# Kernel optimization log

Measured on AMD Instinct MI355X. Metric: run time of the kernel, lower is better.

Reference implementation:

```python
import jax, jax.numpy as jnp
import numpy as np

BINS = 10
LOSS_WEIGHT = 1.0


def setup_inputs() -> dict:
    key = jax.random.key(0)
    k1, k2 = jax.random.split(key)
    B, C = 16384, 1000
    logits = jax.random.normal(k1, (B, C), dtype=jnp.float32)
    target_indices = jax.random.randint(k2, (B,), 0, C)
    return {"logits": logits, "target_indices": target_indices}


def reference(logits, target_indices):
    B, C = logits.shape
    bins = BINS
    target = jax.nn.one_hot(target_indices, C, dtype=logits.dtype)  # [B, C]
    # gradient-norm proxy (detached in the original)
    g = jnp.abs(jax.nn.sigmoid(jax.lax.stop_gradient(logits)) - target)  # [B, C], in [0, 1]
    tot = jnp.asarray(B * C, logits.dtype)  # all label_weights are 1 -> tot = B*C
    # edges are i/bins with last edge bumped by 1e-6, so bin = clip(floor(g*bins), 0, bins-1)
    bin_idx = jnp.clip((g * bins).astype(jnp.int32), 0, bins - 1)  # [B, C]
    counts = jax.ops.segment_sum(
        jnp.ones((B * C,), logits.dtype), bin_idx.reshape(-1), num_segments=bins
    )  # [bins]
    nonempty = counts > 0
    n = jnp.sum(nonempty).astype(logits.dtype)  # number of non-empty bins
    per_bin_w = jnp.where(nonempty, tot / jnp.maximum(counts, 1.0), 0.0)  # [bins]
    weights = per_bin_w[bin_idx] / jnp.maximum(n, 1.0)  # [B, C]
    weights = jax.lax.stop_gradient(weights)
    # binary_cross_entropy_with_logits, elementwise, stable form
    bce = jnp.maximum(logits, 0.0) - logits * target + jnp.log1p(jnp.exp(-jnp.abs(logits)))
    loss = jnp.sum(weights * bce) / tot
    return loss * LOSS_WEIGHT
```

## Files before the change

kernel.cpp:

```cpp
#include <hip/hip_runtime.h>

typedef float v2f __attribute__((ext_vector_type(2)));

namespace {
constexpr int kB = 16384;
constexpr int kC = 1000;
constexpr int kNElem = kB * kC;
constexpr int kNV8 = kNElem / 8;
constexpr int kV8PerRow = kC / 8;
constexpr int kBlocks = 1280;
constexpr int kThreads = 256;
constexpr int kStride = kBlocks * kThreads;
}


__device__ __forceinline__ void ghmc_elem(float L, float& bce, unsigned& bin)
{
    const float kLn2   = 0.6931471805599453f;
    const float kNRLn2 = -1.4426950408889634f;
    const float en  = __builtin_amdgcn_exp2f(kNRLn2 * fabsf(L));
    const float den = 1.f + en;
    const float lg  = __builtin_amdgcn_logf(den);
    const float r   = __builtin_amdgcn_rcpf(den);
    bce = fmaf(lg, kLn2, fmaxf(L, 0.f));
    unsigned babs = (unsigned)(10.f * r);
    babs = babs > 9u ? 9u : babs;
    bin = (L >= 0.f) ? babs : 9u - babs;
}

__device__ __forceinline__ void proc4(const float4 v,
    v2f& a01, v2f& a23, v2f& a45, v2f& a67, v2f& a89,
    unsigned long long& hcnt,
    const v2f C01, const v2f C23, const v2f C45, const v2f C67, const v2f C89)
{
    const float lv[4] = {v.x, v.y, v.z, v.w};
    #pragma unroll
    for (int e = 0; e < 4; ++e) {
        float bce; unsigned bin;
        ghmc_elem(lv[e], bce, bin);
        hcnt += 1ull << (6u * bin);
        const v2f b2 = {bce, bce};
        a01 += __builtin_elementwise_max(b2, C01);
        a23 += __builtin_elementwise_max(b2, C23);
        a45 += __builtin_elementwise_max(b2, C45);
        a67 += __builtin_elementwise_max(b2, C67);
        a89 += __builtin_elementwise_max(b2, C89);
    }
}

__global__ __launch_bounds__(kThreads) void ghmc_main(
    const float* __restrict__ logits,
    const int* __restrict__ tgt,
    float* __restrict__ pf,
    unsigned* __restrict__ pu)
{
    const v2f C01 = {0.0f,        0.10536052f};
    const v2f C23 = {0.22314355f, 0.35667494f};
    const v2f C45 = {0.51082562f, 0.69314718f};
    const v2f C67 = {0.91629073f, 1.20397280f};
    const v2f C89 = {1.60943791f, 2.30258509f};

    v2f a01 = {0.f,0.f}, a23 = {0.f,0.f}, a45 = {0.f,0.f},
        a67 = {0.f,0.f}, a89 = {0.f,0.f};
    unsigned long long hcnt = 0ull;

    const int gid = blockIdx.x * blockDim.x + threadIdx.x;
    const int n = (kNV8 - 1 - gid) / kStride + 1;
    const float4* __restrict__ Lp = reinterpret_cast<const float4*>(logits);

    int i = gid;
    int ib = i + kStride;     if (ib >= kNV8) ib = kNV8 - 1;
    float4 a0 = Lp[2 * i],  a1 = Lp[2 * i + 1];
    float4 b0 = Lp[2 * ib], b1 = Lp[2 * ib + 1];

    for (int k = 0; k < n; ++k) {
        int ic = i + 2 * kStride; if (ic >= kNV8) ic = kNV8 - 1;
        const float4 c0 = Lp[2 * ic], c1 = Lp[2 * ic + 1];

        const int row = i / kV8PerRow;
        const int dt  = tgt[row] - (i - row * kV8PerRow) * 8;

        proc4(a0, a01, a23, a45, a67, a89, hcnt, C01, C23, C45, C67, C89);
        proc4(a1, a01, a23, a45, a67, a89, hcnt, C01, C23, C45, C67, C89);

        if (__builtin_expect((unsigned)dt < 8u, 0)) {
            float L = a0.x;
            L = (dt == 1) ? a0.y : L;
            L = (dt == 2) ? a0.z : L;
            L = (dt == 3) ? a0.w : L;
            L = (dt == 4) ? a1.x : L;
            L = (dt == 5) ? a1.y : L;
            L = (dt == 6) ? a1.z : L;
            L = (dt == 7) ? a1.w : L;
            float bn_; unsigned bnb;
            ghmc_elem(L, bn_, bnb);
            const float bt_ = bn_ - L;
            unsigned babs = (bnb >= 5u) ? bnb : 9u - bnb;
            const unsigned btb = (L <= 0.f) ? babs : 9u - babs;
            hcnt += (1ull << (6u * btb)) - (1ull << (6u * bnb));
            const v2f bn2 = {bn_, bn_}, bt2 = {bt_, bt_};
            a01 += __builtin_elementwise_max(bt2, C01) - __builtin_elementwise_max(bn2, C01);
            a23 += __builtin_elementwise_max(bt2, C23) - __builtin_elementwise_max(bn2, C23);
            a45 += __builtin_elementwise_max(bt2, C45) - __builtin_elementwise_max(bn2, C45);
            a67 += __builtin_elementwise_max(bt2, C67) - __builtin_elementwise_max(bn2, C67);
            a89 += __builtin_elementwise_max(bt2, C89) - __builtin_elementwise_max(bn2, C89);
        }

        a0 = b0; a1 = b1; b0 = c0; b1 = c1;
        i += kStride;
    }

    unsigned long long lo = 0ull, hi = 0ull;
    #pragma unroll
    for (int k = 0; k < 5; ++k) {
        lo += ((hcnt >> (6 * k))       & 63ull) << (12 * k);
        hi += ((hcnt >> (6 * (k + 5))) & 63ull) << (12 * k);
    }
    float r10[10] = {a01.x, a01.y, a23.x, a23.y, a45.x, a45.y, a67.x, a67.y, a89.x, a89.y};
    #pragma unroll
    for (int off = 32; off > 0; off >>= 1) {
        #pragma unroll
        for (int k = 0; k < 10; ++k) r10[k] += __shfl_down(r10[k], off);
        lo += __shfl_down(lo, off);
        hi += __shfl_down(hi, off);
    }

    __shared__ float              sf[4][10];
    __shared__ unsigned long long sc[4][2];
    const int wave = threadIdx.x >> 6;
    const int lane = threadIdx.x & 63;
    if (lane == 0) {
        #pragma unroll
        for (int k = 0; k < 10; ++k) sf[wave][k] = r10[k];
        sc[wave][0] = lo; sc[wave][1] = hi;
    }
    __syncthreads();
    const int t = threadIdx.x;
    if (t < 10) {
        pf[t * kBlocks + blockIdx.x] = sf[0][t] + sf[1][t] + sf[2][t] + sf[3][t];
    } else if (t < 20) {
        const int b = t - 10;
        const int half = (b < 5) ? 0 : 1;
        const int sh = 12 * (b < 5 ? b : b - 5);
        unsigned s = 0;
        #pragma unroll
        for (int w = 0; w < 4; ++w) s += (unsigned)((sc[w][half] >> sh) & 4095ull);
        pu[b * kBlocks + blockIdx.x] = s;
    }
}

__global__ __launch_bounds__(640) void ghmc_reduce(
    const float* __restrict__ pf,
    const unsigned* __restrict__ pu,
    float* __restrict__ out)
{
    const int wave = threadIdx.x >> 6;
    const int lane = threadIdx.x & 63;

    double   fs = 0.0;
    unsigned cs = 0u;
    for (int b = lane; b < kBlocks; b += 64) {
        fs += (double)pf[wave * kBlocks + b];
        cs += pu[wave * kBlocks + b];
    }
    #pragma unroll
    for (int off = 32; off > 0; off >>= 1) {
        fs += __shfl_down(fs, off);
        cs += __shfl_down(cs, off);
    }

    __shared__ double   sF[10];
    __shared__ unsigned sC[10];
    if (lane == 0) { sF[wave] = fs; sC[wave] = cs; }
    __syncthreads();

    if (threadIdx.x == 0) {
        const double cj[10] = {0.0,
            0.10536051565782630, 0.22314355131420976, 0.35667494393873245,
            0.51082562376599072, 0.69314718055994531, 0.91629073187415511,
            1.20397280432593600, 1.60943791243410040, 2.30258509299404570};
        double N[10], cnt[11], cum[11];
        for (int k = 0; k < 10; ++k) N[k] = (double)sC[k];
        cnt[10] = 0.0;
        for (int j = 9; j >= 0; --j) cnt[j] = cnt[j + 1] + N[j];
        cum[10] = 0.0;
        cum[0] = sF[0];
        for (int j = 1; j <= 9; ++j)
            cum[j] = sF[j] - cj[j] * ((double)kNElem - cnt[j]);
        double loss = 0.0, n = 0.0;
        for (int k = 0; k < 10; ++k) {
            if (N[k] > 0.0) { n += 1.0; loss += (cum[k] - cum[k + 1]) / N[k]; }
        }
        out[0] = (float)(loss / (n > 1.0 ? n : 1.0));
    }
}

extern "C" void kernel_launch(void* const* d_in, const int* in_sizes, int n_in,
                              void* d_out, int out_size, void* d_ws, size_t ws_size,
                              hipStream_t stream)
{
    const float* logits = (const float*)d_in[0];
    const int*   tgt    = (const int*)d_in[1];
    float*    pf = (float*)d_ws;
    unsigned* pu = (unsigned*)((char*)d_ws + 10 * kBlocks * 4);
    ghmc_main<<<kBlocks, kThreads, 0, stream>>>(logits, tgt, pf, pu);
    ghmc_reduce<<<1, 640, 0, stream>>>(pf, pu, (float*)d_out);
}
```

Measured before the change: 37.23 us.

## Switch to one coalesced float4 per lane with a deeper prefetch pipeline

The main loop now handles a single float4 per thread per grid-stride step instead of two adjacent float4s. Neighbouring lanes therefore read contiguous 16-byte chunks, and a three-deep register prefetch ring with a 4x unrolled loop keeps more loads in flight. The target-column check moves into the per-float4 routine, so the row and target lookup now runs twice as often. The final reduction kernel also switches to vectorized float4/uint4 loads with a fixed unrolled trip count.

```diff
diff --git a/kernel.cpp b/kernel.cpp
--- a/kernel.cpp
+++ b/kernel.cpp
@@ -6,11 +6,11 @@
 constexpr int kB = 16384;
 constexpr int kC = 1000;
 constexpr int kNElem = kB * kC;
-constexpr int kNV8 = kNElem / 8;
-constexpr int kV8PerRow = kC / 8;
+constexpr int kNV4 = kNElem / 4;
+constexpr int kV4PerRow = kC / 4;
 constexpr int kBlocks = 1280;
 constexpr int kThreads = 256;
-constexpr int kStride = kBlocks * kThreads;
+constexpr int kS = kBlocks * kThreads;
 }
 
 
@@ -28,7 +28,7 @@
     bin = (L >= 0.f) ? babs : 9u - babs;
 }
 
-__device__ __forceinline__ void proc4(const float4 v,
+__device__ __forceinline__ void proc4(const float4 v, int dt,
     v2f& a01, v2f& a23, v2f& a45, v2f& a67, v2f& a89,
     unsigned long long& hcnt,
     const v2f C01, const v2f C23, const v2f C45, const v2f C67, const v2f C89)
@@ -46,6 +46,30 @@
         a67 += __builtin_elementwise_max(b2, C67);
         a89 += __builtin_elementwise_max(b2, C89);
     }
+    if (__builtin_expect((unsigned)dt < 4u, 0)) {
+        float L = v.x;
+        L = (dt == 1) ? v.y : L;
+        L = (dt == 2) ? v.z : L;
+        L = (dt == 3) ? v.w : L;
+        float bn_; unsigned bnb;
+        ghmc_elem(L, bn_, bnb);
+        const float bt_ = bn_ - L;
+        const unsigned babs = (bnb >= 5u) ? bnb : 9u - bnb;
+        const unsigned btb  = (L <= 0.f) ? babs : 9u - babs;
+        hcnt += (1ull << (6u * btb)) - (1ull << (6u * bnb));
+        const v2f bn2 = {bn_, bn_}, bt2 = {bt_, bt_};
+        a01 += __builtin_elementwise_max(bt2, C01) - __builtin_elementwise_max(bn2, C01);
+        a23 += __builtin_elementwise_max(bt2, C23) - __builtin_elementwise_max(bn2, C23);
+        a45 += __builtin_elementwise_max(bt2, C45) - __builtin_elementwise_max(bn2, C45);
+        a67 += __builtin_elementwise_max(bt2, C67) - __builtin_elementwise_max(bn2, C67);
+        a89 += __builtin_elementwise_max(bt2, C89) - __builtin_elementwise_max(bn2, C89);
+    }
+}
+
+__device__ __forceinline__ int dt_for(const int* __restrict__ tgt, int i)
+{
+    const int row = i / kV4PerRow;
+    return tgt[row] - (i - row * kV4PerRow) * 4;
 }
 
 __global__ __launch_bounds__(kThreads) void ghmc_main(
@@ -65,62 +89,46 @@
     unsigned long long hcnt = 0ull;
 
     const int gid = blockIdx.x * blockDim.x + threadIdx.x;
-    const int n = (kNV8 - 1 - gid) / kStride + 1;
+    const int n = (kNV4 - 1 - gid) / kS + 1;
     const float4* __restrict__ Lp = reinterpret_cast<const float4*>(logits);
 
+    auto ld = [&](int idx) {
+        idx = idx < kNV4 ? idx : kNV4 - 1;
+        return Lp[idx];
+    };
+
     int i = gid;
-    int ib = i + kStride;     if (ib >= kNV8) ib = kNV8 - 1;
-    float4 a0 = Lp[2 * i],  a1 = Lp[2 * i + 1];
-    float4 b0 = Lp[2 * ib], b1 = Lp[2 * ib + 1];
-
-    for (int k = 0; k < n; ++k) {
-        int ic = i + 2 * kStride; if (ic >= kNV8) ic = kNV8 - 1;
-        const float4 c0 = Lp[2 * ic], c1 = Lp[2 * ic + 1];
-
-        const int row = i / kV8PerRow;
-        const int dt  = tgt[row] - (i - row * kV8PerRow) * 8;
-
-        proc4(a0, a01, a23, a45, a67, a89, hcnt, C01, C23, C45, C67, C89);
-        proc4(a1, a01, a23, a45, a67, a89, hcnt, C01, C23, C45, C67, C89);
-
-        if (__builtin_expect((unsigned)dt < 8u, 0)) {
-            float L = a0.x;
-            L = (dt == 1) ? a0.y : L;
-            L = (dt == 2) ? a0.z : L;
-            L = (dt == 3) ? a0.w : L;
-            L = (dt == 4) ? a1.x : L;
-            L = (dt == 5) ? a1.y : L;
-            L = (dt == 6) ? a1.z : L;
-            L = (dt == 7) ? a1.w : L;
-            float bn_; unsigned bnb;
-            ghmc_elem(L, bn_, bnb);
-            const float bt_ = bn_ - L;
-            unsigned babs = (bnb >= 5u) ? bnb : 9u - bnb;
-            const unsigned btb = (L <= 0.f) ? babs : 9u - babs;
-            hcnt += (1ull << (6u * btb)) - (1ull << (6u * bnb));
-            const v2f bn2 = {bn_, bn_}, bt2 = {bt_, bt_};
-            a01 += __builtin_elementwise_max(bt2, C01) - __builtin_elementwise_max(bn2, C01);
-            a23 += __builtin_elementwise_max(bt2, C23) - __builtin_elementwise_max(bn2, C23);
-            a45 += __builtin_elementwise_max(bt2, C45) - __builtin_elementwise_max(bn2, C45);
-            a67 += __builtin_elementwise_max(bt2, C67) - __builtin_elementwise_max(bn2, C67);
-            a89 += __builtin_elementwise_max(bt2, C89) - __builtin_elementwise_max(bn2, C89);
-        }
-
-        a0 = b0; a1 = b1; b0 = c0; b1 = c1;
-        i += kStride;
+    float4 q0 = ld(i), q1 = ld(i + kS), q2 = ld(i + 2 * kS);
+
+    int k = 0;
+    for (; k + 4 <= n; k += 4) {
+        float4 q3 = ld(i + 3 * kS);
+        proc4(q0, dt_for(tgt, i),          a01, a23, a45, a67, a89, hcnt, C01, C23, C45, C67, C89);
+        q0 = ld(i + 4 * kS);
+        proc4(q1, dt_for(tgt, i + kS),     a01, a23, a45, a67, a89, hcnt, C01, C23, C45, C67, C89);
+        q1 = ld(i + 5 * kS);
+        proc4(q2, dt_for(tgt, i + 2 * kS), a01, a23, a45, a67, a89, hcnt, C01, C23, C45, C67, C89);
+        q2 = ld(i + 6 * kS);
+        proc4(q3, dt_for(tgt, i + 3 * kS), a01, a23, a45, a67, a89, hcnt, C01, C23, C45, C67, C89);
+        i += 4 * kS;
+    }
+    for (; k < n; ++k) {
+        proc4(q0, dt_for(tgt, i), a01, a23, a45, a67, a89, hcnt, C01, C23, C45, C67, C89);
+        q0 = q1; q1 = q2;
+        i += kS;
     }
 
     unsigned long long lo = 0ull, hi = 0ull;
     #pragma unroll
-    for (int k = 0; k < 5; ++k) {
-        lo += ((hcnt >> (6 * k))       & 63ull) << (12 * k);
-        hi += ((hcnt >> (6 * (k + 5))) & 63ull) << (12 * k);
+    for (int j = 0; j < 5; ++j) {
+        lo += ((hcnt >> (6 * j))       & 63ull) << (12 * j);
+        hi += ((hcnt >> (6 * (j + 5))) & 63ull) << (12 * j);
     }
     float r10[10] = {a01.x, a01.y, a23.x, a23.y, a45.x, a45.y, a67.x, a67.y, a89.x, a89.y};
     #pragma unroll
     for (int off = 32; off > 0; off >>= 1) {
         #pragma unroll
-        for (int k = 0; k < 10; ++k) r10[k] += __shfl_down(r10[k], off);
+        for (int j = 0; j < 10; ++j) r10[j] += __shfl_down(r10[j], off);
         lo += __shfl_down(lo, off);
         hi += __shfl_down(hi, off);
     }
@@ -131,7 +139,7 @@
     const int lane = threadIdx.x & 63;
     if (lane == 0) {
         #pragma unroll
-        for (int k = 0; k < 10; ++k) sf[wave][k] = r10[k];
+        for (int j = 0; j < 10; ++j) sf[wave][j] = r10[j];
         sc[wave][0] = lo; sc[wave][1] = hi;
     }
     __syncthreads();
@@ -157,11 +165,16 @@
     const int wave = threadIdx.x >> 6;
     const int lane = threadIdx.x & 63;
 
+    const float4* pf4 = reinterpret_cast<const float4*>(pf + wave * kBlocks);
+    const uint4*  pu4 = reinterpret_cast<const uint4*>(pu + wave * kBlocks);
     double   fs = 0.0;
     unsigned cs = 0u;
-    for (int b = lane; b < kBlocks; b += 64) {
-        fs += (double)pf[wave * kBlocks + b];
-        cs += pu[wave * kBlocks + b];
+    #pragma unroll
+    for (int it = 0; it < kBlocks / 256; ++it) {
+        const float4 f = pf4[lane + it * 64];
+        const uint4  u = pu4[lane + it * 64];
+        fs += (double)f.x + (double)f.y + (double)f.z + (double)f.w;
+        cs += u.x + u.y + u.z + u.w;
     }
     #pragma unroll
     for (int off = 32; off > 0; off >>= 1) {
@@ -180,7 +193,7 @@
             0.51082562376599072, 0.69314718055994531, 0.91629073187415511,
             1.20397280432593600, 1.60943791243410040, 2.30258509299404570};
         double N[10], cnt[11], cum[11];
-        for (int k = 0; k < 10; ++k) N[k] = (double)sC[k];
+        for (int j = 0; j < 10; ++j) N[j] = (double)sC[j];
         cnt[10] = 0.0;
         for (int j = 9; j >= 0; --j) cnt[j] = cnt[j + 1] + N[j];
         cum[10] = 0.0;
@@ -188,8 +201,8 @@
         for (int j = 1; j <= 9; ++j)
             cum[j] = sF[j] - cj[j] * ((double)kNElem - cnt[j]);
         double loss = 0.0, n = 0.0;
-        for (int k = 0; k < 10; ++k) {
-            if (N[k] > 0.0) { n += 1.0; loss += (cum[k] - cum[k + 1]) / N[k]; }
+        for (int j = 0; j < 10; ++j) {
+            if (N[j] > 0.0) { n += 1.0; loss += (cum[j] - cum[j + 1]) / N[j]; }
         }
         out[0] = (float)(loss / (n > 1.0 ? n : 1.0));
     }
```

New measurement: 31.87 us, median of 2. -14.4%, faster.
